# Kernel tuning notes

Measured on AMD Instinct MI355X. Metric: run time of the kernel, lower is better.

Reference implementation:

```python
import jax, jax.numpy as jnp
import numpy as np

B, C, T = 256, 1, 16384   # batch, input_channels, seq_len
H = C                      # hidden_size == input_channels in this module
OUT = 1                    # output_channels


def setup_inputs() -> dict:
    key = jax.random.key(0)
    ks = jax.random.split(key, 11)
    # PyTorch GRU/Linear init: uniform(-1/sqrt(H), 1/sqrt(H)); H=1 -> (-1, 1)
    u = lambda k, shape, s=1.0: jax.random.uniform(k, shape, jnp.float32, -s, s)
    s_lin = 1.0 / np.sqrt(2 * H).astype(np.float32)
    return {
        "x": jax.random.normal(ks[0], (B, C, T), jnp.float32),
        # layer 0: input size C, per direction [3H, C] / [3H, H] / [3H]
        "w_ih0": u(ks[1], (2, 3 * H, C)),
        "w_hh0": u(ks[2], (2, 3 * H, H)),
        "b_ih0": u(ks[3], (2, 3 * H)),
        "b_hh0": u(ks[4], (2, 3 * H)),
        # layers 1-2: input size 2H (bidirectional concat)
        "w_ih12": u(ks[5], (2, 2, 3 * H, 2 * H)),
        "w_hh12": u(ks[6], (2, 2, 3 * H, H)),
        "b_ih12": u(ks[7], (2, 2, 3 * H)),
        "b_hh12": u(ks[8], (2, 2, 3 * H)),
        # output projection Linear(2H -> OUT)
        "w_out": u(ks[9], (OUT, 2 * H), s_lin),
        "b_out": u(ks[10], (OUT,), s_lin),
    }


def _gru_dir(xs, w_ih, w_hh, b_ih, b_hh, reverse):
    """One GRU direction. xs: [T, B, in] -> ys: [T, B, H] (time-aligned)."""
    h0 = jnp.zeros((xs.shape[1], w_hh.shape[1]), xs.dtype)

    def step(h, x_t):
        gi = x_t @ w_ih.T + b_ih          # [B, 3H]
        gh = h @ w_hh.T + b_hh            # [B, 3H]
        ir, iz, inn = jnp.split(gi, 3, axis=-1)
        hr, hz, hn = jnp.split(gh, 3, axis=-1)
        r = jax.nn.sigmoid(ir + hr)
        z = jax.nn.sigmoid(iz + hz)
        n = jnp.tanh(inn + r * hn)
        h_new = (1.0 - z) * n + z * h
        return h_new, h_new

    _, ys = jax.lax.scan(step, h0, xs, reverse=reverse)
    return ys


def _bidir(xs, w_ih_f, w_hh_f, b_ih_f, b_hh_f, w_ih_b, w_hh_b, b_ih_b, b_hh_b):
    fwd = _gru_dir(xs, w_ih_f, w_hh_f, b_ih_f, b_hh_f, reverse=False)
    bwd = _gru_dir(xs, w_ih_b, w_hh_b, b_ih_b, b_hh_b, reverse=True)
    return jnp.concatenate([fwd, bwd], axis=-1)  # [T, B, 2H]


def reference(x, w_ih0, w_hh0, b_ih0, b_hh0, w_ih12, w_hh12, b_ih12, b_hh12, w_out, b_out):
    xs = jnp.transpose(x, (2, 0, 1))  # [B, C, T] -> [T, B, C]
    xs = _bidir(xs, w_ih0[0], w_hh0[0], b_ih0[0], b_hh0[0],
                w_ih0[1], w_hh0[1], b_ih0[1], b_hh0[1])
    for l in range(2):  # GRU layers 1 and 2 (structurally distinct weights)
        xs = _bidir(xs, w_ih12[l, 0], w_hh12[l, 0], b_ih12[l, 0], b_hh12[l, 0],
                    w_ih12[l, 1], w_hh12[l, 1], b_ih12[l, 1], b_hh12[l, 1])
    y = xs @ w_out.T + b_out          # [T, B, OUT]
    return jnp.transpose(y, (1, 2, 0))  # [B, OUT, T]
```

## Files before the change

kernel.cpp:

```cpp
#include <hip/hip_runtime.h>

#define T_LEN 16384
#define B_SZ  256
#define S_CH  256
#define CL    (T_LEN / S_CH)
#define HALO  64
#define SC    32

__device__ __forceinline__ float ex2(float x)  { return __builtin_amdgcn_exp2f(x); }
__device__ __forceinline__ float rcpf(float x) { return __builtin_amdgcn_rcpf(x); }

__device__ __forceinline__ float gru_step(float h, float preR, float preZ, float preN,
                                          float UR, float UZ, float UN2, float DN2)
{
    float er  = ex2(fmaf(h, UR, preR));
    float ez  = ex2(fmaf(h, UZ, preZ));
    float r   = rcpf(1.0f + er);
    float z   = rcpf(1.0f + ez);
    float hn2 = fmaf(h, UN2, DN2);
    float en  = ex2(fmaf(r, hn2, preN));
    float n   = fmaf(-2.0f, rcpf(1.0f + en), 1.0f);
    float omz = 1.0f - z;
    float zh  = z * h;
    return fmaf(n, omz, zh);
}

__global__ void __launch_bounds__(256) k_tr(const float* __restrict__ x, float* __restrict__ xT)
{
    __shared__ float tile[64][65];
    const int b0 = (blockIdx.x & 3) * 64;
    const int t0 = (blockIdx.x >> 2) * 64;
    const int c4 = threadIdx.x & 15;
    const int r  = threadIdx.x >> 4;
    #pragma unroll
    for (int i = 0; i < 4; ++i) {
        int row = r + 16 * i;
        float4 v = ((const float4*)x)[(size_t)(b0 + row) * (T_LEN / 4) + t0 / 4 + c4];
        tile[c4*4+0][row] = v.x; tile[c4*4+1][row] = v.y;
        tile[c4*4+2][row] = v.z; tile[c4*4+3][row] = v.w;
    }
    __syncthreads();
    #pragma unroll
    for (int i = 0; i < 4; ++i) {
        int trow = r + 16 * i;
        float4 v = make_float4(tile[trow][c4*4+0], tile[trow][c4*4+1],
                               tile[trow][c4*4+2], tile[trow][c4*4+3]);
        ((float4*)xT)[(size_t)(t0 + trow) * (B_SZ / 4) + b0 / 4 + c4] = v;
    }
}

template<bool REV>
__device__ void scan0(const float* __restrict__ xT,
                      const float* __restrict__ wih, const float* __restrict__ whh,
                      const float* __restrict__ bih, const float* __restrict__ bhh,
                      float* __restrict__ out, int b, int s)
{
    const int d = REV ? 1 : 0;
    const float L2E = 1.4426950408889634f;
    const float WR  = -L2E * wih[d*3+0];
    const float WZ  = -L2E * wih[d*3+1];
    const float WN  =  2.0f*L2E * wih[d*3+2];
    const float UR  = -L2E * whh[d*3+0];
    const float UZ  = -L2E * whh[d*3+1];
    const float UN2 =  2.0f*L2E * whh[d*3+2];
    const float CR  = -L2E * (bih[d*3+0] + bhh[d*3+0]);
    const float CZ  = -L2E * (bih[d*3+1] + bhh[d*3+1]);
    const float CN  =  2.0f*L2E * bih[d*3+2];
    const float DN2 =  2.0f*L2E * bhh[d*3+2];

    const int warm   = min(HALO, REV ? (T_LEN - (s + 1) * CL) : (s * CL));
    const int nsteps = warm + CL;
    const int t0     = REV ? ((s + 1) * CL - 1 + warm) : (s * CL - warm);

    const float* px = xT + b;
    float* po = out + (REV ? B_SZ : 0) + b;

    float xA[SC], xB[SC];
    float h = 0.0f;

#define LD0(F, base_) { int base = (base_); \
    _Pragma("unroll") for (int k = 0; k < SC; ++k) { \
      int t = REV ? (t0 - (base + k)) : (t0 + (base + k)); \
      F[k] = px[t * B_SZ]; } \
    __builtin_amdgcn_sched_barrier(0); }

#define CS0(F, base_) { int base = (base_); bool st = (base >= warm); \
    _Pragma("unroll") for (int k = 0; k < SC; ++k) { \
      float xv = F[k]; \
      h = gru_step(h, fmaf(xv, WR, CR), fmaf(xv, WZ, CZ), fmaf(xv, WN, CN), \
                   UR, UZ, UN2, DN2); \
      if (st) { int t = REV ? (t0 - (base + k)) : (t0 + (base + k)); \
                po[t * (2 * B_SZ)] = h; } } }

    LD0(xA, 0);
    const int nsup = nsteps / SC;
    for (int i = 0; i < nsup; i += 2) {
        LD0(xB, min((i + 1) * SC, nsteps - SC));
        CS0(xA, i * SC);
        LD0(xA, min((i + 2) * SC, nsteps - SC));
        CS0(xB, (i + 1) * SC);
    }
#undef LD0
#undef CS0
}

template<bool REV>
__device__ void scan12(const float* __restrict__ in,
                       const float* __restrict__ wih, const float* __restrict__ whh,
                       const float* __restrict__ bih, const float* __restrict__ bhh,
                       float* __restrict__ out, int b, int s)
{
    const int d = REV ? 1 : 0;
    const float L2E = 1.4426950408889634f;
    const float WR0 = -L2E * wih[(d*3+0)*2+0], WR1 = -L2E * wih[(d*3+0)*2+1];
    const float WZ0 = -L2E * wih[(d*3+1)*2+0], WZ1 = -L2E * wih[(d*3+1)*2+1];
    const float WN0 =  2.0f*L2E * wih[(d*3+2)*2+0], WN1 = 2.0f*L2E * wih[(d*3+2)*2+1];
    const float UR  = -L2E * whh[d*3+0];
    const float UZ  = -L2E * whh[d*3+1];
    const float UN2 =  2.0f*L2E * whh[d*3+2];
    const float CR  = -L2E * (bih[d*3+0] + bhh[d*3+0]);
    const float CZ  = -L2E * (bih[d*3+1] + bhh[d*3+1]);
    const float CN  =  2.0f*L2E * bih[d*3+2];
    const float DN2 =  2.0f*L2E * bhh[d*3+2];

    const int warm   = min(HALO, REV ? (T_LEN - (s + 1) * CL) : (s * CL));
    const int nsteps = warm + CL;
    const int t0     = REV ? ((s + 1) * CL - 1 + warm) : (s * CL - warm);

    const float* pf = in + b;
    const float* pg = in + B_SZ + b;
    float* po = out + (REV ? B_SZ : 0) + b;

    float fA[SC], gA[SC], fB[SC], gB[SC];
    float h = 0.0f;

#define LD12(F, G, base_) { int base = (base_); \
    _Pragma("unroll") for (int k = 0; k < SC; ++k) { \
      int t = REV ? (t0 - (base + k)) : (t0 + (base + k)); \
      F[k] = pf[t * (2 * B_SZ)]; G[k] = pg[t * (2 * B_SZ)]; } \
    __builtin_amdgcn_sched_barrier(0); }

#define CS12(F, G, base_) { int base = (base_); bool st = (base >= warm); \
    _Pragma("unroll") for (int k = 0; k < SC; ++k) { \
      float a = F[k], c = G[k]; \
      float pr = fmaf(a, WR0, fmaf(c, WR1, CR)); \
      float pz = fmaf(a, WZ0, fmaf(c, WZ1, CZ)); \
      float pn = fmaf(a, WN0, fmaf(c, WN1, CN)); \
      h = gru_step(h, pr, pz, pn, UR, UZ, UN2, DN2); \
      if (st) { int t = REV ? (t0 - (base + k)) : (t0 + (base + k)); \
                po[t * (2 * B_SZ)] = h; } } }

    LD12(fA, gA, 0);
    const int nsup = nsteps / SC;
    for (int i = 0; i < nsup; i += 2) {
        LD12(fB, gB, min((i + 1) * SC, nsteps - SC));
        CS12(fA, gA, i * SC);
        LD12(fA, gA, min((i + 2) * SC, nsteps - SC));
        CS12(fB, gB, (i + 1) * SC);
    }
#undef LD12
#undef CS12
}

__device__ __forceinline__ void decode_blk(int blk, int tid, int& b, int& s, int& dir)
{
    int xcd = blk & 7;
    int j   = blk >> 3;
    int sl  = j & 31;
    int bg  = (j >> 5) & 3;
    dir     = j >> 7;
    s       = xcd * 32 + sl;
    b       = bg * 64 + tid;
}

__global__ void __launch_bounds__(64) k_scan0g(const float* __restrict__ xT,
                                               const float* __restrict__ wih,
                                               const float* __restrict__ whh,
                                               const float* __restrict__ bih,
                                               const float* __restrict__ bhh,
                                               float* __restrict__ out)
{
    int b, s, dir;
    decode_blk(blockIdx.x, threadIdx.x, b, s, dir);
    if (dir == 0) scan0<false>(xT, wih, whh, bih, bhh, out, b, s);
    else          scan0<true >(xT, wih, whh, bih, bhh, out, b, s);
}

__global__ void __launch_bounds__(64) k_scan12g(const float* __restrict__ in,
                                                const float* __restrict__ wih,
                                                const float* __restrict__ whh,
                                                const float* __restrict__ bih,
                                                const float* __restrict__ bhh,
                                                float* __restrict__ out)
{
    int b, s, dir;
    decode_blk(blockIdx.x, threadIdx.x, b, s, dir);
    if (dir == 0) scan12<false>(in, wih, whh, bih, bhh, out, b, s);
    else          scan12<true >(in, wih, whh, bih, bhh, out, b, s);
}

__global__ void __launch_bounds__(256) k_proj(const float* __restrict__ h2,
                                              const float* __restrict__ wo,
                                              const float* __restrict__ bo,
                                              float* __restrict__ y)
{
    __shared__ float tile[64][65];
    const int b0 = (blockIdx.x & 3) * 64;
    const int t0 = (blockIdx.x >> 2) * 64;
    const float wf = wo[0], wb = wo[1], bias = bo[0];
    const int bl = threadIdx.x & 63;
    const int tg = threadIdx.x >> 6;
    #pragma unroll
    for (int i = 0; i < 16; ++i) {
        int tl = tg * 16 + i;
        int t  = t0 + tl;
        float f = h2[(size_t)t * (2 * B_SZ) + b0 + bl];
        float g = h2[(size_t)t * (2 * B_SZ) + B_SZ + b0 + bl];
        tile[bl][tl] = fmaf(wf, f, fmaf(wb, g, bias));
    }
    __syncthreads();
    const int c4 = threadIdx.x & 15;
    const int r  = threadIdx.x >> 4;
    #pragma unroll
    for (int i = 0; i < 4; ++i) {
        int brow = r + 16 * i;
        float4 v = make_float4(tile[brow][c4*4+0], tile[brow][c4*4+1],
                               tile[brow][c4*4+2], tile[brow][c4*4+3]);
        ((float4*)y)[(size_t)(b0 + brow) * (T_LEN / 4) + t0 / 4 + c4] = v;
    }
}

extern "C" void kernel_launch(void* const* d_in, const int* in_sizes, int n_in,
                              void* d_out, int out_size, void* d_ws, size_t ws_size,
                              hipStream_t stream)
{
    (void)in_sizes; (void)n_in; (void)out_size; (void)ws_size;
    const float* x      = (const float*)d_in[0];
    const float* w_ih0  = (const float*)d_in[1];
    const float* w_hh0  = (const float*)d_in[2];
    const float* b_ih0  = (const float*)d_in[3];
    const float* b_hh0  = (const float*)d_in[4];
    const float* w_ih12 = (const float*)d_in[5];
    const float* w_hh12 = (const float*)d_in[6];
    const float* b_ih12 = (const float*)d_in[7];
    const float* b_hh12 = (const float*)d_in[8];
    const float* w_out  = (const float*)d_in[9];
    const float* b_out  = (const float*)d_in[10];
    float* y = (float*)d_out;

    float* ws    = (float*)d_ws;
    float* xT    = ws;
    float* l0out = ws + (size_t)2 * B_SZ * T_LEN;
    float* l1out = ws;
    float* l2out = ws + (size_t)2 * B_SZ * T_LEN;

    const int nblk = 8 * S_CH;
    k_tr     <<<1024, 256, 0, stream>>>(x, xT);
    k_scan0g <<<nblk, 64, 0, stream>>>(xT,    w_ih0,       w_hh0,      b_ih0,      b_hh0,      l0out);
    k_scan12g<<<nblk, 64, 0, stream>>>(l0out, w_ih12 + 0,  w_hh12 + 0, b_ih12 + 0, b_hh12 + 0, l1out);
    k_scan12g<<<nblk, 64, 0, stream>>>(l1out, w_ih12 + 12, w_hh12 + 6, b_ih12 + 6, b_hh12 + 6, l2out);
    k_proj   <<<1024, 256, 0, stream>>>(l2out, w_out, b_out, y);
}
```

Baseline: 164.2 us.

## Store inter-layer GRU activations in fp16 and batch stores per chunk

The layer-0 and layer-1 scan outputs now go to workspace as half precision, and the next layer converts them back to float on load. This halves the memory traffic of the intermediate activations. Stores are now buffered per chunk and written after the recurrence loop, and the chunk size drops from 32 to 16 to ease register pressure. The fp16 rounding of the hidden states may add numerical error across the three layers.

New measurement: 153.1 us. 6.8% less time.

```diff
diff --git a/kernel.cpp b/kernel.cpp
--- a/kernel.cpp
+++ b/kernel.cpp
@@ -1,14 +1,20 @@
 #include <hip/hip_runtime.h>
+#include <hip/hip_fp16.h>
 
 #define T_LEN 16384
 #define B_SZ  256
 #define S_CH  256
 #define CL    (T_LEN / S_CH)
 #define HALO  64
-#define SC    32
+#define SC    16
 
 __device__ __forceinline__ float ex2(float x)  { return __builtin_amdgcn_exp2f(x); }
 __device__ __forceinline__ float rcpf(float x) { return __builtin_amdgcn_rcpf(x); }
+
+__device__ __forceinline__ float ld_cvt(const float* p)  { return *p; }
+__device__ __forceinline__ float ld_cvt(const __half* p) { return __half2float(*p); }
+__device__ __forceinline__ void  st_cvt(float* p, float v)  { *p = v; }
+__device__ __forceinline__ void  st_cvt(__half* p, float v) { *p = __float2half_rn(v); }
 
 __device__ __forceinline__ float gru_step(float h, float preR, float preZ, float preN,
                                           float UR, float UZ, float UN2, float DN2)
@@ -53,7 +59,7 @@
 __device__ void scan0(const float* __restrict__ xT,
                       const float* __restrict__ wih, const float* __restrict__ whh,
                       const float* __restrict__ bih, const float* __restrict__ bhh,
-                      float* __restrict__ out, int b, int s)
+                      __half* __restrict__ out, int b, int s)
 {
     const int d = REV ? 1 : 0;
     const float L2E = 1.4426950408889634f;
@@ -73,7 +79,7 @@
     const int t0     = REV ? ((s + 1) * CL - 1 + warm) : (s * CL - warm);
 
     const float* px = xT + b;
-    float* po = out + (REV ? B_SZ : 0) + b;
+    __half* po = out + (REV ? B_SZ : 0) + b;
 
     float xA[SC], xB[SC];
     float h = 0.0f;
@@ -84,13 +90,15 @@
       F[k] = px[t * B_SZ]; } \
     __builtin_amdgcn_sched_barrier(0); }
 
-#define CS0(F, base_) { int base = (base_); bool st = (base >= warm); \
+#define CS0(F, base_) { int base = (base_); float ov[SC]; \
     _Pragma("unroll") for (int k = 0; k < SC; ++k) { \
       float xv = F[k]; \
       h = gru_step(h, fmaf(xv, WR, CR), fmaf(xv, WZ, CZ), fmaf(xv, WN, CN), \
-                   UR, UZ, UN2, DN2); \
-      if (st) { int t = REV ? (t0 - (base + k)) : (t0 + (base + k)); \
-                po[t * (2 * B_SZ)] = h; } } }
+                   UR, UZ, UN2, DN2); ov[k] = h; } \
+    if (base >= warm) { \
+      _Pragma("unroll") for (int k = 0; k < SC; ++k) { \
+        int t = REV ? (t0 - (base + k)) : (t0 + (base + k)); \
+        st_cvt(po + t * (2 * B_SZ), ov[k]); } } }
 
     LD0(xA, 0);
     const int nsup = nsteps / SC;
@@ -104,11 +112,11 @@
 #undef CS0
 }
 
-template<bool REV>
-__device__ void scan12(const float* __restrict__ in,
+template<bool REV, typename TIN, typename TOUT>
+__device__ void scan12(const TIN* __restrict__ in,
                        const float* __restrict__ wih, const float* __restrict__ whh,
                        const float* __restrict__ bih, const float* __restrict__ bhh,
-                       float* __restrict__ out, int b, int s)
+                       TOUT* __restrict__ out, int b, int s)
 {
     const int d = REV ? 1 : 0;
     const float L2E = 1.4426950408889634f;
@@ -127,9 +135,9 @@
     const int nsteps = warm + CL;
     const int t0     = REV ? ((s + 1) * CL - 1 + warm) : (s * CL - warm);
 
-    const float* pf = in + b;
-    const float* pg = in + B_SZ + b;
-    float* po = out + (REV ? B_SZ : 0) + b;
+    const TIN* pf = in + b;
+    const TIN* pg = in + B_SZ + b;
+    TOUT* po = out + (REV ? B_SZ : 0) + b;
 
     float fA[SC], gA[SC], fB[SC], gB[SC];
     float h = 0.0f;
@@ -137,18 +145,20 @@
 #define LD12(F, G, base_) { int base = (base_); \
     _Pragma("unroll") for (int k = 0; k < SC; ++k) { \
       int t = REV ? (t0 - (base + k)) : (t0 + (base + k)); \
-      F[k] = pf[t * (2 * B_SZ)]; G[k] = pg[t * (2 * B_SZ)]; } \
+      F[k] = ld_cvt(pf + t * (2 * B_SZ)); G[k] = ld_cvt(pg + t * (2 * B_SZ)); } \
     __builtin_amdgcn_sched_barrier(0); }
 
-#define CS12(F, G, base_) { int base = (base_); bool st = (base >= warm); \
+#define CS12(F, G, base_) { int base = (base_); float ov[SC]; \
     _Pragma("unroll") for (int k = 0; k < SC; ++k) { \
       float a = F[k], c = G[k]; \
       float pr = fmaf(a, WR0, fmaf(c, WR1, CR)); \
       float pz = fmaf(a, WZ0, fmaf(c, WZ1, CZ)); \
       float pn = fmaf(a, WN0, fmaf(c, WN1, CN)); \
-      h = gru_step(h, pr, pz, pn, UR, UZ, UN2, DN2); \
-      if (st) { int t = REV ? (t0 - (base + k)) : (t0 + (base + k)); \
-                po[t * (2 * B_SZ)] = h; } } }
+      h = gru_step(h, pr, pz, pn, UR, UZ, UN2, DN2); ov[k] = h; } \
+    if (base >= warm) { \
+      _Pragma("unroll") for (int k = 0; k < SC; ++k) { \
+        int t = REV ? (t0 - (base + k)) : (t0 + (base + k)); \
+        st_cvt(po + t * (2 * B_SZ), ov[k]); } } }
 
     LD12(fA, gA, 0);
     const int nsup = nsteps / SC;
@@ -178,7 +188,7 @@
                                                const float* __restrict__ whh,
                                                const float* __restrict__ bih,
                                                const float* __restrict__ bhh,
-                                               float* __restrict__ out)
+                                               __half* __restrict__ out)
 {
     int b, s, dir;
     decode_blk(blockIdx.x, threadIdx.x, b, s, dir);
@@ -186,12 +196,25 @@
     else          scan0<true >(xT, wih, whh, bih, bhh, out, b, s);
 }
 
-__global__ void __launch_bounds__(64) k_scan12g(const float* __restrict__ in,
-                                                const float* __restrict__ wih,
-                                                const float* __restrict__ whh,
-                                                const float* __restrict__ bih,
-                                                const float* __restrict__ bhh,
-                                                float* __restrict__ out)
+__global__ void __launch_bounds__(64) k_scan1g(const __half* __restrict__ in,
+                                               const float* __restrict__ wih,
+                                               const float* __restrict__ whh,
+                                               const float* __restrict__ bih,
+                                               const float* __restrict__ bhh,
+                                               __half* __restrict__ out)
+{
+    int b, s, dir;
+    decode_blk(blockIdx.x, threadIdx.x, b, s, dir);
+    if (dir == 0) scan12<false>(in, wih, whh, bih, bhh, out, b, s);
+    else          scan12<true >(in, wih, whh, bih, bhh, out, b, s);
+}
+
+__global__ void __launch_bounds__(64) k_scan2g(const __half* __restrict__ in,
+                                               const float* __restrict__ wih,
+                                               const float* __restrict__ whh,
+                                               const float* __restrict__ bih,
+                                               const float* __restrict__ bhh,
+                                               float* __restrict__ out)
 {
     int b, s, dir;
     decode_blk(blockIdx.x, threadIdx.x, b, s, dir);
@@ -248,16 +271,17 @@
     const float* b_out  = (const float*)d_in[10];
     float* y = (float*)d_out;
 
-    float* ws    = (float*)d_ws;
-    float* xT    = ws;
-    float* l0out = ws + (size_t)2 * B_SZ * T_LEN;
-    float* l1out = ws;
-    float* l2out = ws + (size_t)2 * B_SZ * T_LEN;
+    char* ws = (char*)d_ws;
+    const size_t NN = (size_t)2 * B_SZ * T_LEN;
+    float*  xT    = (float*)ws;
+    __half* l0out = (__half*)(ws + NN * 4);
+    __half* l1out = (__half*)ws;
+    float*  l2out = (float*)(ws + NN * 4);
 
     const int nblk = 8 * S_CH;
-    k_tr     <<<1024, 256, 0, stream>>>(x, xT);
-    k_scan0g <<<nblk, 64, 0, stream>>>(xT,    w_ih0,       w_hh0,      b_ih0,      b_hh0,      l0out);
-    k_scan12g<<<nblk, 64, 0, stream>>>(l0out, w_ih12 + 0,  w_hh12 + 0, b_ih12 + 0, b_hh12 + 0, l1out);
-    k_scan12g<<<nblk, 64, 0, stream>>>(l1out, w_ih12 + 12, w_hh12 + 6, b_ih12 + 6, b_hh12 + 6, l2out);
-    k_proj   <<<1024, 256, 0, stream>>>(l2out, w_out, b_out, y);
-}
+    k_tr    <<<1024, 256, 0, stream>>>(x, xT);
+    k_scan0g<<<nblk, 64, 0, stream>>>(xT,    w_ih0,       w_hh0,      b_ih0,      b_hh0,      l0out);
+    k_scan1g<<<nblk, 64, 0, stream>>>(l0out, w_ih12 + 0,  w_hh12 + 0, b_ih12 + 0, b_hh12 + 0, l1out);
+    k_scan2g<<<nblk, 64, 0, stream>>>(l1out, w_ih12 + 12, w_hh12 + 6, b_ih12 + 6, b_hh12 + 6, l2out);
+    k_proj  <<<1024, 256, 0, stream>>>(l2out, w_out, b_out, y);
+}
```
